# Performance work log

Measured on AMD Instinct MI355X. Metric: run time of the kernel, lower is better.

## Reference

```python
import jax, jax.numpy as jnp
import numpy as np

B, T, E, U, V = 4096, 80, 100, 64, 10000

def setup_inputs() -> dict:
    key = jax.random.key(0)
    ks = jax.random.split(key, 10)
    s = lambda *sh: 0.05
    return {
        "tokens": jax.random.randint(ks[0], (B, T), 0, V, dtype=jnp.int32),
        "emb": jax.random.normal(ks[1], (V, E), jnp.float32) * 0.05,
        "k0": jax.random.normal(ks[2], (E, 4 * U), jnp.float32) * 0.05,
        "r0": jax.random.normal(ks[3], (U, 4 * U), jnp.float32) * 0.05,
        "b0": jnp.zeros((4 * U,), jnp.float32),
        "k1": jax.random.normal(ks[4], (E, 4 * U), jnp.float32) * 0.05,
        "r1": jax.random.normal(ks[5], (U, 4 * U), jnp.float32) * 0.05,
        "b1": jnp.zeros((4 * U,), jnp.float32),
        "Wd": jax.random.normal(ks[6], (U, 1), jnp.float32) * 0.05,
        "bd": jnp.zeros((1,), jnp.float32),
    }

def _lstm_cell(h, c, xt, k, r, b):
    # keras LSTMCell gate order: i, f, g(cell candidate), o
    z = xt @ k + h @ r + b  # [B, 4U]
    i, f, g, o = jnp.split(z, 4, axis=-1)
    c_new = jax.nn.sigmoid(f) * c + jax.nn.sigmoid(i) * jnp.tanh(g)
    h_new = jax.nn.sigmoid(o) * jnp.tanh(c_new)
    return h_new, c_new

def reference(tokens, emb, k0, r0, b0, k1, r1, b1, Wd, bd):
    x = emb[tokens]                 # [B, T, E]
    xs = jnp.swapaxes(x, 0, 1)      # [T, B, E] for scan over time
    zeros = jnp.zeros((tokens.shape[0], U), x.dtype)
    init = (zeros, zeros, zeros, zeros)  # h0, c0, h1, c1

    def step(state, xt):
        h0, c0, h1, c1 = state
        h0, c0 = _lstm_cell(h0, c0, xt, k0, r0, b0)
        # NOTE: original feeds the raw embedded word (not out0) to cell 1
        h1, c1 = _lstm_cell(h1, c1, xt, k1, r1, b1)
        return (h0, c0, h1, c1), None

    (h0, c0, h1, c1), _ = jax.lax.scan(step, init, xs)
    logits = h1 @ Wd + bd           # [B, 1]
    return jax.nn.sigmoid(logits)
```

## Files before the change

### kernel.cpp

```cpp
#include <hip/hip_runtime.h>
#include <hip/hip_bf16.h>

#define B_  4096
#define T_  80
#define E_  100
#define U_  64
#define G_  256
#define V_  10000

#define ROWS 8
#define S_H  72
#define TP   81
#define ZR   68
#define AS   136

typedef __attribute__((ext_vector_type(8))) __bf16 bf16x8;
typedef __attribute__((ext_vector_type(4))) __bf16 bf16x4;
typedef __attribute__((ext_vector_type(2))) __bf16 bf16x2;
typedef __attribute__((ext_vector_type(4))) float  floatx4;

__device__ __forceinline__ float sigmoidf_(float x) {
    return __fdividef(1.f, 1.f + __expf(-x));
}

__device__ __forceinline__ float cell_(float zi, float zf, float zg, float zo,
                                       float& c) {
    float ei = __expf(-zi);
    float eg = __expf(2.f * zg);
    float Ai = 1.f + ei, Bg = 1.f + eg;
    float rig = __builtin_amdgcn_rcpf(Ai * Bg);
    float term1 = (rig * Bg) * fmaf(-2.f, rig * Ai, 1.f);
    float sf = __builtin_amdgcn_rcpf(1.f + __expf(-zf));
    float cn = fmaf(sf, c, term1);
    float eo = __expf(-zo);
    float ec = __expf(2.f * cn);
    float Ao = 1.f + eo, Bc = 1.f + ec;
    float roc = __builtin_amdgcn_rcpf(Ao * Bc);
    float hn = (roc * Bc) * fmaf(-2.f, roc * Ao, 1.f);
    c = cn;
    return hn;
}

__device__ __forceinline__ void lds_barrier_() {
    asm volatile("s_waitcnt lgkmcnt(0)\n\ts_barrier" ::: "memory");
}

__global__ __launch_bounds__(256) void embk_kernel(const float* __restrict__ emb,
                                                   const float* __restrict__ k1,
                                                   const float* __restrict__ b1,
                                                   float* __restrict__ embk) {
    __shared__ __bf16 aLDS[64 * AS];

    const int tid  = threadIdx.x;
    const int lane = tid & 63;
    const int w    = tid >> 6;
    const int n    = lane & 15;
    const int kg   = lane >> 4;
    const int v0   = blockIdx.x * 64;
    const int nrows = min(64, V_ - v0);

    for (int i = tid; i < 64 * 28; i += 256) {
        int r = i / 28, e = 100 + (i - r * 28);
        aLDS[r * AS + e] = (__bf16)0.f;
    }
    for (int i = tid; i < nrows * E_; i += 256) {
        int r = i / E_, e = i - r * E_;
        aLDS[r * AS + e] = (__bf16)emb[(long)v0 * E_ + i];
    }

    bf16x8 bfr[4][4];
#pragma unroll
    for (int ct = 0; ct < 4; ++ct)
#pragma unroll
        for (int kc = 0; kc < 4; ++kc) {
            bf16x8 s;
#pragma unroll
            for (int jj = 0; jj < 8; ++jj) {
                int k = kc * 32 + kg * 8 + jj;
                s[jj] = (k < E_) ? (__bf16)k1[k * G_ + w * 64 + ct * 16 + n]
                                 : (__bf16)0.f;
            }
            bfr[ct][kc] = s;
        }

    float bv0 = b1[w * 64 +  0 + n];
    float bv1 = b1[w * 64 + 16 + n];
    float bv2 = b1[w * 64 + 32 + n];
    float bv3 = b1[w * 64 + 48 + n];

    __syncthreads();

#pragma unroll
    for (int mt = 0; mt < 4; ++mt) {
        const __bf16* ab = aLDS + (mt * 16 + n) * AS + kg * 8;
        bf16x8 a0 = *(const bf16x8*)(ab + 0 * 32);
        bf16x8 a1 = *(const bf16x8*)(ab + 1 * 32);
        bf16x8 a2 = *(const bf16x8*)(ab + 2 * 32);
        bf16x8 a3 = *(const bf16x8*)(ab + 3 * 32);
#pragma unroll
        for (int ct = 0; ct < 4; ++ct) {
            float bv = (ct == 0) ? bv0 : (ct == 1) ? bv1 : (ct == 2) ? bv2 : bv3;
            floatx4 acc = {bv, bv, bv, bv};
            acc = __builtin_amdgcn_mfma_f32_16x16x32_bf16(a0, bfr[ct][0], acc, 0, 0, 0);
            acc = __builtin_amdgcn_mfma_f32_16x16x32_bf16(a1, bfr[ct][1], acc, 0, 0, 0);
            acc = __builtin_amdgcn_mfma_f32_16x16x32_bf16(a2, bfr[ct][2], acc, 0, 0, 0);
            acc = __builtin_amdgcn_mfma_f32_16x16x32_bf16(a3, bfr[ct][3], acc, 0, 0, 0);
#pragma unroll
            for (int r = 0; r < 4; ++r) {
                int v = v0 + mt * 16 + kg * 4 + r;
                if (v < V_) embk[(long)v * G_ + w * 64 + ct * 16 + n] = acc[r];
            }
        }
    }
}

__global__ __launch_bounds__(256, 2) void lstm_kernel(const int*   __restrict__ tokens,
                                                      const float* __restrict__ embk,
                                                      const float* __restrict__ r1,
                                                      const float* __restrict__ Wd,
                                                      const float* __restrict__ bd,
                                                      float* __restrict__ out) {
    __shared__ int    tokLDS[ROWS * TP];
    __shared__ __bf16 hbuf[2][16 * S_H];
    __shared__ float  zw[4][16 * ZR];

    const int tid  = threadIdx.x;
    const int lane = tid & 63;
    const int w    = tid >> 6;
    const int n    = lane & 15;
    const int kg   = lane >> 4;
    const int bb   = blockIdx.x * ROWS;
    const int row8 = n & 7;

    const int grow = lane & 7;
    const int u8   = lane >> 3;
    const int gp   = (u8 + grow) & 7;
    const int gu   = gp * 2;

    for (int i = tid; i < ROWS * T_; i += 256) {
        int r = i / T_, t = i - r * T_;
        tokLDS[r * TP + t] = tokens[bb * T_ + i];
    }
    for (int i = tid; i < 2 * 16 * S_H; i += 256) (&hbuf[0][0])[i] = (__bf16)0.f;

    bf16x8 afr[4][2];
#pragma unroll
    for (int ct = 0; ct < 4; ++ct)
#pragma unroll
        for (int kc = 0; kc < 2; ++kc) {
            bf16x8 s;
#pragma unroll
            for (int jj = 0; jj < 8; ++jj)
                s[jj] = (__bf16)r1[(kc * 32 + kg * 8 + jj) * G_ + ct * 64 + w * 16 + n];
            afr[ct][kc] = s;
        }

    float c0 = 0.f, c1 = 0.f;

    __syncthreads();

    floatx4 xkb[2][4];
#pragma unroll
    for (int s = 0; s < 2; ++s) {
        const float* base = embk + (long)tokLDS[row8 * TP + s] * G_ + w * 16 + kg * 4;
#pragma unroll
        for (int ct = 0; ct < 4; ++ct)
            xkb[s][ct] = *(const floatx4*)(base + ct * 64);
    }

    float* zme = zw[w];

    auto step = [&](int t, int sel) {
        const __bf16* hb = hbuf[sel ^ 1];
        bf16x8 b0 = *(const bf16x8*)(hb + n * S_H + kg * 8);
        bf16x8 b1 = *(const bf16x8*)(hb + n * S_H + 32 + kg * 8);

        floatx4 acc[4];
#pragma unroll
        for (int ct = 0; ct < 4; ++ct) {
            floatx4 a = xkb[sel][ct];
            a = __builtin_amdgcn_mfma_f32_16x16x32_bf16(afr[ct][0], b0, a, 0, 0, 0);
            a = __builtin_amdgcn_mfma_f32_16x16x32_bf16(afr[ct][1], b1, a, 0, 0, 0);
            acc[ct] = a;
        }

        {
            const int tt = (t + 2 < T_) ? (t + 2) : (T_ - 1);
            const float* base = embk + (long)tokLDS[row8 * TP + tt] * G_ + w * 16 + kg * 4;
#pragma unroll
            for (int ct = 0; ct < 4; ++ct)
                xkb[sel][ct] = *(const floatx4*)(base + ct * 64);
        }

#pragma unroll
        for (int r = 0; r < 4; ++r) {
            floatx4 v = {acc[0][r], acc[1][r], acc[2][r], acc[3][r]};
            *(floatx4*)(zme + n * ZR + (kg * 4 + r) * 4) = v;
        }
        __builtin_amdgcn_wave_barrier();

        const float* zc = zme + grow * ZR + gu * 4;
        floatx4 z0 = *(const floatx4*)(zc);
        floatx4 z1 = *(const floatx4*)(zc + 4);

        float hn0 = cell_(z0[0], z0[1], z0[2], z0[3], c0);
        float hn1 = cell_(z1[0], z1[1], z1[2], z1[3], c1);

        bf16x2 hv; hv[0] = (__bf16)hn0; hv[1] = (__bf16)hn1;
        *(bf16x2*)(&hbuf[sel][0] + grow * S_H + w * 16 + gu) = hv;

        lds_barrier_();
    };

    for (int t = 0; t < T_; t += 2) {
        step(t,     0);
        step(t + 1, 1);
    }

    if (tid < ROWS) {
        const __bf16* hb = hbuf[1] + tid * S_H;
        float s = bd[0];
#pragma unroll
        for (int u = 0; u < U_; ++u) s = fmaf((float)hb[u], Wd[u], s);
        out[bb + tid] = sigmoidf_(s);
    }
}

extern "C" void kernel_launch(void* const* d_in, const int* in_sizes, int n_in,
                              void* d_out, int out_size, void* d_ws, size_t ws_size,
                              hipStream_t stream) {
    const int*   tokens = (const int*)  d_in[0];
    const float* emb    = (const float*)d_in[1];
    const float* k1     = (const float*)d_in[5];
    const float* r1     = (const float*)d_in[6];
    const float* b1     = (const float*)d_in[7];
    const float* Wd     = (const float*)d_in[8];
    const float* bd     = (const float*)d_in[9];
    float*       out    = (float*)d_out;

    float* embk = (float*)d_ws;

    embk_kernel<<<(V_ + 63) / 64, 256, 0, stream>>>(emb, k1, b1, embk);
    lstm_kernel<<<B_ / ROWS, 256, 0, stream>>>(tokens, embk, r1, Wd, bd, out);
}
```

Measured before the change: 160.8 us.

## Use single-wave blocks computing all gates per lane, removing LDS z transpose

Each block is now one wavefront handling 16 batch rows and all 256 gate columns via 16 MFMA tiles, laid out so each lane holds i,f,g,o for the same units in registers. This eliminates the LDS staging of gate preactivations and the block-wide barrier each timestep. In exchange, each wave does four times the MFMA and cell work serially, the grid has fewer waves per CU, and register pressure rises.

```diff
diff --git a/kernel.cpp b/kernel.cpp
--- a/kernel.cpp
+++ b/kernel.cpp
@@ -8,15 +8,12 @@
 #define G_  256
 #define V_  10000
 
-#define ROWS 8
-#define S_H  72
 #define TP   81
-#define ZR   68
+#define HS   72
 #define AS   136
 
 typedef __attribute__((ext_vector_type(8))) __bf16 bf16x8;
 typedef __attribute__((ext_vector_type(4))) __bf16 bf16x4;
-typedef __attribute__((ext_vector_type(2))) __bf16 bf16x2;
 typedef __attribute__((ext_vector_type(4))) float  floatx4;
 
 __device__ __forceinline__ float sigmoidf_(float x) {
@@ -41,10 +38,6 @@
     return hn;
 }
 
-__device__ __forceinline__ void lds_barrier_() {
-    asm volatile("s_waitcnt lgkmcnt(0)\n\ts_barrier" ::: "memory");
-}
-
 __global__ __launch_bounds__(256) void embk_kernel(const float* __restrict__ emb,
                                                    const float* __restrict__ k1,
                                                    const float* __restrict__ b1,
@@ -114,115 +107,94 @@
     }
 }
 
-__global__ __launch_bounds__(256, 2) void lstm_kernel(const int*   __restrict__ tokens,
-                                                      const float* __restrict__ embk,
-                                                      const float* __restrict__ r1,
-                                                      const float* __restrict__ Wd,
-                                                      const float* __restrict__ bd,
-                                                      float* __restrict__ out) {
-    __shared__ int    tokLDS[ROWS * TP];
-    __shared__ __bf16 hbuf[2][16 * S_H];
-    __shared__ float  zw[4][16 * ZR];
-
-    const int tid  = threadIdx.x;
-    const int lane = tid & 63;
-    const int w    = tid >> 6;
+__global__ __launch_bounds__(64, 1) void lstm_kernel(const int*   __restrict__ tokens,
+                                                     const float* __restrict__ embk,
+                                                     const float* __restrict__ r1,
+                                                     const float* __restrict__ Wd,
+                                                     const float* __restrict__ bd,
+                                                     float* __restrict__ out) {
+    __shared__ int    tokLDS[16 * TP];
+    __shared__ __bf16 hX[16 * HS];
+
+    const int lane = threadIdx.x;
     const int n    = lane & 15;
     const int kg   = lane >> 4;
-    const int bb   = blockIdx.x * ROWS;
-    const int row8 = n & 7;
-
-    const int grow = lane & 7;
-    const int u8   = lane >> 3;
-    const int gp   = (u8 + grow) & 7;
-    const int gu   = gp * 2;
-
-    for (int i = tid; i < ROWS * T_; i += 256) {
+    const int bb   = blockIdx.x * 16;
+
+    for (int i = lane; i < 16 * T_; i += 64) {
         int r = i / T_, t = i - r * T_;
         tokLDS[r * TP + t] = tokens[bb * T_ + i];
     }
-    for (int i = tid; i < 2 * 16 * S_H; i += 256) (&hbuf[0][0])[i] = (__bf16)0.f;
-
-    bf16x8 afr[4][2];
-#pragma unroll
-    for (int ct = 0; ct < 4; ++ct)
+    for (int i = lane; i < 16 * HS; i += 64) hX[i] = (__bf16)0.f;
+
+    bf16x8 afr[16][2];
+#pragma unroll
+    for (int ct = 0; ct < 16; ++ct)
 #pragma unroll
         for (int kc = 0; kc < 2; ++kc) {
             bf16x8 s;
 #pragma unroll
             for (int jj = 0; jj < 8; ++jj)
-                s[jj] = (__bf16)r1[(kc * 32 + kg * 8 + jj) * G_ + ct * 64 + w * 16 + n];
+                s[jj] = (__bf16)r1[(kc * 32 + kg * 8 + jj) * G_ + ct * 16 + n];
             afr[ct][kc] = s;
         }
 
-    float c0 = 0.f, c1 = 0.f;
-
-    __syncthreads();
-
-    floatx4 xkb[2][4];
-#pragma unroll
-    for (int s = 0; s < 2; ++s) {
-        const float* base = embk + (long)tokLDS[row8 * TP + s] * G_ + w * 16 + kg * 4;
-#pragma unroll
-        for (int ct = 0; ct < 4; ++ct)
-            xkb[s][ct] = *(const floatx4*)(base + ct * 64);
-    }
-
-    float* zme = zw[w];
-
-    auto step = [&](int t, int sel) {
-        const __bf16* hb = hbuf[sel ^ 1];
-        bf16x8 b0 = *(const bf16x8*)(hb + n * S_H + kg * 8);
-        bf16x8 b1 = *(const bf16x8*)(hb + n * S_H + 32 + kg * 8);
-
-        floatx4 acc[4];
-#pragma unroll
-        for (int ct = 0; ct < 4; ++ct) {
-            floatx4 a = xkb[sel][ct];
-            a = __builtin_amdgcn_mfma_f32_16x16x32_bf16(afr[ct][0], b0, a, 0, 0, 0);
-            a = __builtin_amdgcn_mfma_f32_16x16x32_bf16(afr[ct][1], b1, a, 0, 0, 0);
-            acc[ct] = a;
+    float c[4][4];
+#pragma unroll
+    for (int q = 0; q < 4; ++q)
+#pragma unroll
+        for (int r = 0; r < 4; ++r) c[q][r] = 0.f;
+
+    floatx4 xc[16];
+    {
+        const float* base = embk + (long)tokLDS[n * TP + 0] * G_ + kg * 4;
+#pragma unroll
+        for (int ct = 0; ct < 16; ++ct)
+            xc[ct] = *(const floatx4*)(base + ct * 16);
+    }
+
+    for (int t = 0; t < T_; ++t) {
+        bf16x8 hb0 = *(const bf16x8*)(hX + n * HS + kg * 8);
+        bf16x8 hb1 = *(const bf16x8*)(hX + n * HS + 32 + kg * 8);
+
+        floatx4 z[16];
+#pragma unroll
+        for (int ct = 0; ct < 16; ++ct) {
+            floatx4 a = xc[ct];
+            a = __builtin_amdgcn_mfma_f32_16x16x32_bf16(afr[ct][0], hb0, a, 0, 0, 0);
+            a = __builtin_amdgcn_mfma_f32_16x16x32_bf16(afr[ct][1], hb1, a, 0, 0, 0);
+            z[ct] = a;
         }
 
         {
-            const int tt = (t + 2 < T_) ? (t + 2) : (T_ - 1);
-            const float* base = embk + (long)tokLDS[row8 * TP + tt] * G_ + w * 16 + kg * 4;
-#pragma unroll
-            for (int ct = 0; ct < 4; ++ct)
-                xkb[sel][ct] = *(const floatx4*)(base + ct * 64);
-        }
-
-#pragma unroll
-        for (int r = 0; r < 4; ++r) {
-            floatx4 v = {acc[0][r], acc[1][r], acc[2][r], acc[3][r]};
-            *(floatx4*)(zme + n * ZR + (kg * 4 + r) * 4) = v;
-        }
-        __builtin_amdgcn_wave_barrier();
-
-        const float* zc = zme + grow * ZR + gu * 4;
-        floatx4 z0 = *(const floatx4*)(zc);
-        floatx4 z1 = *(const floatx4*)(zc + 4);
-
-        float hn0 = cell_(z0[0], z0[1], z0[2], z0[3], c0);
-        float hn1 = cell_(z1[0], z1[1], z1[2], z1[3], c1);
-
-        bf16x2 hv; hv[0] = (__bf16)hn0; hv[1] = (__bf16)hn1;
-        *(bf16x2*)(&hbuf[sel][0] + grow * S_H + w * 16 + gu) = hv;
-
-        lds_barrier_();
-    };
-
-    for (int t = 0; t < T_; t += 2) {
-        step(t,     0);
-        step(t + 1, 1);
-    }
-
-    if (tid < ROWS) {
-        const __bf16* hb = hbuf[1] + tid * S_H;
-        float s = bd[0];
-#pragma unroll
-        for (int u = 0; u < U_; ++u) s = fmaf((float)hb[u], Wd[u], s);
-        out[bb + tid] = sigmoidf_(s);
+            const int tt = (t + 1 < T_) ? (t + 1) : (T_ - 1);
+            const float* base = embk + (long)tokLDS[n * TP + tt] * G_ + kg * 4;
+#pragma unroll
+            for (int ct = 0; ct < 16; ++ct)
+                xc[ct] = *(const floatx4*)(base + ct * 16);
+        }
+
+#pragma unroll
+        for (int q = 0; q < 4; ++q) {
+            bf16x4 hv;
+#pragma unroll
+            for (int r = 0; r < 4; ++r) {
+                float hn = cell_(z[q][r], z[4 + q][r], z[8 + q][r], z[12 + q][r],
+                                 c[q][r]);
+                hv[r] = (__bf16)hn;
+            }
+            *(bf16x4*)(hX + n * HS + 16 * q + 4 * kg) = hv;
+        }
+    }
+
+    {
+        float s = 0.f;
+#pragma unroll
+        for (int u = 0; u < 16; ++u)
+            s = fmaf((float)hX[n * HS + kg * 16 + u], Wd[kg * 16 + u], s);
+        s += __shfl_down(s, 32);
+        s += __shfl_down(s, 16);
+        if (lane < 16) out[bb + n] = sigmoidf_(s + bd[0]);
     }
 }
 
@@ -241,5 +213,5 @@
     float* embk = (float*)d_ws;
 
     embk_kernel<<<(V_ + 63) / 64, 256, 0, stream>>>(emb, k1, b1, embk);
-    lstm_kernel<<<B_ / ROWS, 256, 0, stream>>>(tokens, embk, r1, Wd, bd, out);
-}
+    lstm_kernel<<<B_ / 16, 64, 0, stream>>>(tokens, embk, r1, Wd, bd, out);
+}
```

Measured after the change: 192.1 us. 1.2x slower.
